# Kernel optimization log

Hardware: AMD Instinct MI355X
Metric: run time of the kernel (lower is better)

The kernel has to match this reference:

```python
import jax, jax.numpy as jnp
import numpy as np

B, N, D = 2, 2048, 1024
H = 16
HD = D // H  # 64
N_CTX = 256


def setup_inputs() -> dict:
    key = jax.random.key(0)
    ks = jax.random.split(key, 10)
    x = jax.random.normal(ks[0], (B, N, D), dtype=jnp.float32)
    ctx_ppr = jax.random.uniform(ks[1], (N_CTX,), dtype=jnp.float32, minval=1e-4, maxval=1.0)
    ctx_trust = jax.random.uniform(ks[2], (N_CTX,), dtype=jnp.float32)
    attn_mask = jax.random.randint(ks[3], (N, N), 0, 2).astype(jnp.bool_)
    # parameters (nn.Linear convention: y = x @ W.T + b)
    s_in = 1.0 / np.sqrt(D)
    W_in = jax.random.uniform(ks[4], (3 * D, D), dtype=jnp.float32, minval=-s_in, maxval=s_in)
    b_in = jax.random.uniform(ks[5], (3 * D,), dtype=jnp.float32, minval=-s_in, maxval=s_in)
    W_out = jax.random.uniform(ks[6], (D, D), dtype=jnp.float32, minval=-s_in, maxval=s_in)
    b_out = jax.random.uniform(ks[7], (D,), dtype=jnp.float32, minval=-s_in, maxval=s_in)
    log_ppr_alpha = jnp.ones((1,), jnp.float32) * 0.1
    trust_scale = jnp.ones((1,), jnp.float32) * 0.1
    return {"x": x, "ctx_ppr": ctx_ppr, "ctx_trust": ctx_trust, "n_ctx": N_CTX,
            "attn_mask": attn_mask, "W_in": W_in, "b_in": b_in,
            "W_out": W_out, "b_out": b_out,
            "log_ppr_alpha": log_ppr_alpha, "trust_scale": trust_scale}


def reference(x, ctx_ppr, ctx_trust, n_ctx, attn_mask, W_in, b_in, W_out, b_out,
              log_ppr_alpha, trust_scale):
    Bx, Nx, Dx = x.shape
    scale = HD ** -0.5
    qkv = x @ W_in.T + b_in  # [B,N,3D]
    q, k, v = jnp.split(qkv, 3, axis=-1)
    q = q.reshape(Bx, Nx, H, HD).transpose(0, 2, 1, 3)  # [B,H,N,d]
    k = k.reshape(Bx, Nx, H, HD).transpose(0, 2, 1, 3)
    v = v.reshape(Bx, Nx, H, HD).transpose(0, 2, 1, 3)
    if n_ctx > 0:
        gate = jax.nn.sigmoid(trust_scale[0] * ctx_trust)  # [n_ctx]
        gate_full = jnp.concatenate([gate, jnp.ones(Nx - n_ctx, x.dtype)])
        v = v * gate_full[None, None, :, None]
    logits = jnp.einsum('bhqd,bhkd->bhqk', q, k) * scale
    if n_ctx > 0:
        bias = log_ppr_alpha[0] * jnp.log(jnp.clip(ctx_ppr, 1e-8, None))
        col_bias = jnp.concatenate([bias, jnp.zeros(Nx - n_ctx, x.dtype)])
        logits = logits + col_bias[None, None, None, :]
    logits = jnp.where(attn_mask[None, None, :, :], -jnp.inf, logits)
    weights = jax.nn.softmax(logits, axis=-1)
    out = jnp.einsum('bhqk,bhkd->bhqd', weights, v)
    out = out.transpose(0, 2, 1, 3).reshape(Bx, Nx, Dx)
    return out @ W_out.T + b_out
```

## Files before the change

kernel.cpp:

```cpp
#include <hip/hip_runtime.h>
#include <hip/hip_bf16.h>
#include <math.h>

#define B_   2
#define N_   2048
#define D_   1024
#define H_   16
#define TD_  3072
#define LOG2E 1.44269504088896340736f
#define SCALE_Q (0.125f * LOG2E)

typedef short  bf16x8 __attribute__((ext_vector_type(8)));
typedef _Float16 f16x8 __attribute__((ext_vector_type(8)));
typedef float  f32x4  __attribute__((ext_vector_type(4)));
typedef float  f32x16 __attribute__((ext_vector_type(16)));

#define MFMA16(a, b, c)   __builtin_amdgcn_mfma_f32_16x16x32_bf16(a, b, c, 0, 0, 0)
#define MFMA32B(a, b, c)  __builtin_amdgcn_mfma_f32_32x32x16_bf16(a, b, c, 0, 0, 0)
#define MFMA32H(a, b, c)  __builtin_amdgcn_mfma_f32_32x32x16_f16(a, b, c, 0, 0, 0)

__device__ __forceinline__ ushort f2bf(float f) {
    union { float f; unsigned u; } v; v.f = f;
    unsigned r = (v.u + 0x7fffu + ((v.u >> 16) & 1u)) >> 16;
    return (ushort)r;
}
__device__ __forceinline__ unsigned pkrtz(float a, float b) {
    typedef __fp16 h2 __attribute__((ext_vector_type(2)));
    union { h2 h; unsigned u; } c;
    c.h = __builtin_amdgcn_cvt_pkrtz(a, b);
    return c.u;
}
__device__ __forceinline__ void async16(const void* g, void* l) {
    __builtin_amdgcn_global_load_lds(
        (const __attribute__((address_space(1))) unsigned*)g,
        (__attribute__((address_space(3))) unsigned*)l, 16, 0, 0);
}

__global__ __launch_bounds__(256) void preprocess(
    const float* __restrict__ x, const float* __restrict__ W_in,
    const float* __restrict__ W_out, const float* __restrict__ ctx_ppr,
    const float* __restrict__ log_alpha, const int* __restrict__ n_ctx_p,
    const int* __restrict__ mask,
    ushort* __restrict__ xb, ushort* __restrict__ wib, ushort* __restrict__ wob,
    float* __restrict__ biasrow, unsigned* __restrict__ maskbits)
{
    const int J0 = 1048576, J1 = 786432, J2 = 262144, JM = 131072, JB = 2048;
    int t = blockIdx.x * 256 + threadIdx.x;
    if (t < J0 + J1 + J2) {
        const float* src; ushort* dst; int i = t;
        if (i < J0)           { src = x;      dst = xb;  }
        else if (i < J0 + J1) { i -= J0;      src = W_in;  dst = wib; }
        else                  { i -= J0 + J1; src = W_out; dst = wob; }
        float4 v = ((const float4*)src)[i];
        ushort4 o;
        o.x = f2bf(v.x); o.y = f2bf(v.y); o.z = f2bf(v.z); o.w = f2bf(v.w);
        ((ushort4*)dst)[i] = o;
    } else if (t < J0 + J1 + J2 + JM) {
        int i = t - (J0 + J1 + J2);
        const int4* m = (const int4*)(mask + (size_t)i * 32);
        unsigned bits = 0u;
        #pragma unroll
        for (int j = 0; j < 8; ++j) {
            int4 w = m[j];
            bits |= (w.x != 0 ? 1u : 0u) << (j * 4 + 0);
            bits |= (w.y != 0 ? 1u : 0u) << (j * 4 + 1);
            bits |= (w.z != 0 ? 1u : 0u) << (j * 4 + 2);
            bits |= (w.w != 0 ? 1u : 0u) << (j * 4 + 3);
        }
        maskbits[i] = bits;
    } else if (t < J0 + J1 + J2 + JM + JB) {
        int k = t - (J0 + J1 + J2 + JM);
        int nc = n_ctx_p[0];
        float bv = 0.f;
        if (k < nc) bv = log_alpha[0] * __log2f(fmaxf(ctx_ppr[k], 1e-8f));
        biasrow[k] = bv;
    }
}

template<int BCOL, int MODE>
__global__ __launch_bounds__(256) void gemm_bt(
    const ushort* __restrict__ A, const ushort* __restrict__ Bw,
    const float* __restrict__ bias, float* __restrict__ Cout,
    ushort* __restrict__ qkout, _Float16* __restrict__ vTout,
    int Ncol, int K,
    const float* __restrict__ ctx_trust, const float* __restrict__ trust_scale,
    const int* __restrict__ n_ctx_p)
{
    constexpr int NT = BCOL / 32;
    __shared__ ushort tA[128 * 32];
    __shared__ ushort tB[BCOL * 32];
    const int tid = threadIdx.x;
    const int lane = tid & 63, wv = tid >> 6;
    const int ln = lane & 15, kg = lane >> 4;
    const int rh = wv >> 1, ch = wv & 1;
    const int row0 = blockIdx.y * 128, col0 = blockIdx.x * BCOL;

    int offA[4], offB[NT];
    #pragma unroll
    for (int i = 0; i < 4; ++i) {
        int ra = rh * 64 + i * 16 + ln;
        offA[i] = ra * 32 + ((kg ^ ((ra >> 1) & 3)) << 3);
    }
    #pragma unroll
    for (int i = 0; i < NT; ++i) {
        int rb = ch * (BCOL / 2) + i * 16 + ln;
        offB[i] = rb * 32 + ((kg ^ ((rb >> 1) & 3)) << 3);
    }
    f32x4 acc[4][NT];
    #pragma unroll
    for (int i = 0; i < 4; ++i)
        #pragma unroll
        for (int j = 0; j < NT; ++j) acc[i][j] = (f32x4){0.f, 0.f, 0.f, 0.f};

    for (int kt = 0; kt < K; kt += 32) {
        __syncthreads();
        #pragma unroll
        for (int r2 = 0; r2 < 2; ++r2) {
            int g = r2 * 256 + tid;
            int row = g >> 2;
            int srck = ((g & 3) ^ ((row >> 1) & 3)) << 3;
            async16(A + (size_t)(row0 + row) * K + kt + srck, &tA[g * 8]);
        }
        #pragma unroll
        for (int r2 = 0; r2 < BCOL / 64; ++r2) {
            int g = r2 * 256 + tid;
            int row = g >> 2;
            int srck = ((g & 3) ^ ((row >> 1) & 3)) << 3;
            async16(Bw + (size_t)(col0 + row) * K + kt + srck, &tB[g * 8]);
        }
        __syncthreads();
        bf16x8 af[4], bfr[NT];
        #pragma unroll
        for (int i = 0; i < 4; ++i)  af[i]  = *(const bf16x8*)&tA[offA[i]];
        #pragma unroll
        for (int i = 0; i < NT; ++i) bfr[i] = *(const bf16x8*)&tB[offB[i]];
        #pragma unroll
        for (int mt = 0; mt < 4; ++mt)
            #pragma unroll
            for (int nt = 0; nt < NT; ++nt)
                acc[mt][nt] = MFMA16(af[mt], bfr[nt], acc[mt][nt]);
    }

    const int nctx = n_ctx_p ? n_ctx_p[0] : 0;
    const float ts = trust_scale ? trust_scale[0] : 0.f;
    #pragma unroll
    for (int nt = 0; nt < NT; ++nt) {
        int col = col0 + ch * (BCOL / 2) + nt * 16 + ln;
        float bv = bias[col];
        #pragma unroll
        for (int mt = 0; mt < 4; ++mt) {
            int rbase = row0 + rh * 64 + mt * 16 + kg * 4;
            f32x4 a = acc[mt][nt];
            if (MODE == 0) {
                #pragma unroll
                for (int reg = 0; reg < 4; ++reg)
                    Cout[(size_t)(rbase + reg) * Ncol + col] = a[reg] + bv;
            } else {
                if (col < D_) {
                    #pragma unroll
                    for (int reg = 0; reg < 4; ++reg)
                        qkout[(size_t)(rbase + reg) * 2048 + col] =
                            f2bf((a[reg] + bv) * SCALE_Q);
                } else if (col < 2 * D_) {
                    #pragma unroll
                    for (int reg = 0; reg < 4; ++reg)
                        qkout[(size_t)(rbase + reg) * 2048 + col] = f2bf(a[reg] + bv);
                } else {
                    int vc = col - 2 * D_;
                    int hh = vc >> 6, dim = vc & 63;
                    int bb = rbase >> 11, nbase = rbase & (N_ - 1);
                    ushort4 o;
                    #pragma unroll
                    for (int reg = 0; reg < 4; ++reg) {
                        float v = a[reg] + bv;
                        int n = nbase + reg;
                        if (n < nctx) {
                            float g = 1.f / (1.f + __expf(-ts * ctx_trust[n]));
                            v *= g;
                        }
                        _Float16 hv = (_Float16)v;
                        ((ushort*)&o)[reg] = *(ushort*)&hv;
                    }
                    *(ushort4*)&vTout[((size_t)(bb * 16 + hh) * 64 + dim) * 2048 + nbase] = o;
                }
            }
        }
    }
}

__global__ __launch_bounds__(256) void attn(
    const ushort* __restrict__ qkb,
    const _Float16* __restrict__ vT,
    const unsigned* __restrict__ maskbits,
    const float* __restrict__ biasrow,
    const int* __restrict__ n_ctx_p,
    ushort* __restrict__ attb)
{
    __shared__ ushort   Kt[2][64 * 64];
    __shared__ _Float16 Vt[2][64 * 64];
    const int tid = threadIdx.x;
    const int lane = tid & 63, wv = tid >> 6;
    const int q31 = lane & 31, hi = lane >> 5;
    const int b = blockIdx.y >> 4, h = blockIdx.y & 15;
    const int q0w = blockIdx.x * 128 + wv * 32;
    const int nctx = n_ctx_p[0];

    bf16x8 qf[4];
    {
        const ushort* qrow = qkb + (size_t)(b * N_ + q0w + q31) * 2048 + h * 64;
        #pragma unroll
        for (int ks = 0; ks < 4; ++ks)
            qf[ks] = *(const bf16x8*)(qrow + ks * 16 + hi * 8);
    }
    const size_t kgbase = (size_t)(b * N_) * 2048 + 1024 + h * 64;
    const _Float16* vbase = vT + (size_t)((b * 16 + h) * 64) * 2048;

    f32x16 O[2];
    O[0] = (f32x16)(0.f); O[1] = (f32x16)(0.f);
    float lrun = 0.f;

    {
        #pragma unroll
        for (int r2 = 0; r2 < 2; ++r2) {
            int g = r2 * 256 + tid; int row = g >> 3; int sg = (g & 7) ^ (row & 7);
            async16(qkb + kgbase + (size_t)row * 2048 + sg * 8, &Kt[0][g * 8]);
        }
        #pragma unroll
        for (int r2 = 0; r2 < 2; ++r2) {
            int g = r2 * 256 + tid; int row = g >> 3; int sg = (g & 7) ^ (row & 7);
            async16(vbase + (size_t)row * 2048 + sg * 8, &Vt[0][g * 8]);
        }
    }

    const int swz = q31 & 7;
    for (int ci = 0; ci < 32; ++ci) {
        const int c0 = ci * 64;
        __syncthreads();
        if (ci < 31) {
            const int c1 = c0 + 64, nb = (ci + 1) & 1;
            #pragma unroll
            for (int r2 = 0; r2 < 2; ++r2) {
                int g = r2 * 256 + tid; int row = g >> 3; int sg = (g & 7) ^ (row & 7);
                async16(qkb + kgbase + (size_t)(c1 + row) * 2048 + sg * 8, &Kt[nb][g * 8]);
            }
            #pragma unroll
            for (int r2 = 0; r2 < 2; ++r2) {
                int g = r2 * 256 + tid; int row = g >> 3; int sg = (g & 7) ^ (row & 7);
                async16(vbase + (size_t)row * 2048 + c1 + sg * 8, &Vt[nb][g * 8]);
            }
        }
        const ushort*   KT = Kt[ci & 1];
        const _Float16* VT = Vt[ci & 1];

        f32x16 S[2];
        S[0] = (f32x16)(0.f); S[1] = (f32x16)(0.f);
        #pragma unroll
        for (int t = 0; t < 2; ++t) {
            const int rbase = (t * 32 + q31) * 64;
            #pragma unroll
            for (int ks = 0; ks < 4; ++ks) {
                bf16x8 kf = *(const bf16x8*)&KT[rbase + (((ks * 2 + hi) ^ swz) << 3)];
                S[t] = MFMA32B(kf, qf[ks], S[t]);
            }
        }

        uint2 mw = *(const uint2*)&maskbits[(size_t)(q0w + q31) * 64 + ci * 2];
        unsigned msh[2] = { mw.x >> (hi * 4), mw.y >> (hi * 4) };
        unsigned pk[2][8];
        float lsum = 0.f;
        const bool has_bias = (c0 < nctx);
        #pragma unroll
        for (int t = 0; t < 2; ++t) {
            float p[16];
            #pragma unroll
            for (int g = 0; g < 4; ++g) {
                f32x4 bb = (f32x4){0.f, 0.f, 0.f, 0.f};
                if (has_bias)
                    bb = *(const f32x4*)&biasrow[c0 + t * 32 + g * 8 + hi * 4];
                #pragma unroll
                for (int r = 0; r < 4; ++r) {
                    const int reg = g * 4 + r;
                    const int br = r + 8 * g;
                    float s = S[t][reg] + bb[r] - 4.f;
                    s = ((msh[t] >> br) & 1u) ? -1e30f : s;
                    p[reg] = __builtin_exp2f(s);
                }
            }
            float l0 = (p[0] + p[1]) + (p[2] + p[3]);
            float l1 = (p[4] + p[5]) + (p[6] + p[7]);
            float l2 = (p[8] + p[9]) + (p[10] + p[11]);
            float l3 = (p[12] + p[13]) + (p[14] + p[15]);
            lsum += (l0 + l1) + (l2 + l3);
            #pragma unroll
            for (int i = 0; i < 8; ++i)
                pk[t][i] = pkrtz(p[2 * i], p[2 * i + 1]);
        }
        lrun += lsum;

        #pragma unroll
        for (int ks = 0; ks < 4; ++ks) {
            const int t = ks >> 1, lo4 = (ks & 1) * 4;
            unsigned u0 = pk[t][lo4 + 0], u1 = pk[t][lo4 + 1];
            unsigned u2 = pk[t][lo4 + 2], u3 = pk[t][lo4 + 3];
            unsigned own0 = hi ? u2 : u0, own1 = hi ? u3 : u1;
            unsigned snd0 = hi ? u0 : u2, snd1 = hi ? u1 : u3;
            unsigned rv0 = (unsigned)__shfl_xor((int)snd0, 32);
            unsigned rv1 = (unsigned)__shfl_xor((int)snd1, 32);
            union { f16x8 v; unsigned u[4]; } frag;
            frag.u[0] = hi ? rv0 : own0;
            frag.u[1] = hi ? rv1 : own1;
            frag.u[2] = hi ? own0 : rv0;
            frag.u[3] = hi ? own1 : rv1;
            #pragma unroll
            for (int t2 = 0; t2 < 2; ++t2) {
                const int vb = (t2 * 32 + q31) * 64;
                union { f16x8 v; int4 i; } vf;
                vf.i = *(const int4*)&VT[vb + (((ks * 2 + hi) ^ swz) << 3)];
                O[t2] = MFMA32H(vf.v, frag.v, O[t2]);
            }
        }
    }

    float l = lrun + __shfl_xor(lrun, 32);
    float inv = 1.f / l;
    ushort* orow = attb + (size_t)(b * N_ + q0w + q31) * 1024 + h * 64;
    #pragma unroll
    for (int t = 0; t < 2; ++t)
        #pragma unroll
        for (int g = 0; g < 4; ++g) {
            ushort4 o;
            #pragma unroll
            for (int r = 0; r < 4; ++r)
                ((ushort*)&o)[r] = f2bf(O[t][g * 4 + r] * inv);
            *(ushort4*)&orow[t * 32 + g * 8 + hi * 4] = o;
        }
}

extern "C" void kernel_launch(void* const* d_in, const int* in_sizes, int n_in,
                              void* d_out, int out_size, void* d_ws, size_t ws_size,
                              hipStream_t stream)
{
    const float* x         = (const float*)d_in[0];
    const float* ctx_ppr   = (const float*)d_in[1];
    const float* ctx_trust = (const float*)d_in[2];
    const int*   n_ctx_p   = (const int*)d_in[3];
    const int*   attn_mask = (const int*)d_in[4];
    const float* W_in      = (const float*)d_in[5];
    const float* b_in      = (const float*)d_in[6];
    const float* W_out     = (const float*)d_in[7];
    const float* b_out     = (const float*)d_in[8];
    const float* log_alpha = (const float*)d_in[9];
    const float* trust_sc  = (const float*)d_in[10];
    float* out = (float*)d_out;

    char* ws = (char*)d_ws;
    ushort*    xb       = (ushort*)ws;    ws += (size_t)4096 * 1024 * 2;
    ushort*    wib      = (ushort*)ws;    ws += (size_t)3072 * 1024 * 2;
    ushort*    wob      = (ushort*)ws;    ws += (size_t)1024 * 1024 * 2;
    ushort*    qkb      = (ushort*)ws;    ws += (size_t)4096 * 2048 * 2;
    _Float16*  vT       = (_Float16*)ws;  ws += (size_t)2048 * 2048 * 2;
    ushort*    attbuf   = (ushort*)ws;    ws += (size_t)4096 * 1024 * 2;
    float*     biasrow  = (float*)ws;     ws += 2048 * 4;
    unsigned*  maskbits = (unsigned*)ws;  ws += (size_t)2048 * 64 * 4;

    hipLaunchKernelGGL(preprocess, dim3(8712), dim3(256), 0, stream,
                       x, W_in, W_out, ctx_ppr, log_alpha, n_ctx_p, attn_mask,
                       xb, wib, wob, biasrow, maskbits);

    hipLaunchKernelGGL((gemm_bt<128, 1>), dim3(24, 32), dim3(256), 0, stream,
                       xb, wib, b_in, (float*)nullptr, qkb, vT, TD_, 1024,
                       ctx_trust, trust_sc, n_ctx_p);

    hipLaunchKernelGGL(attn, dim3(16, 32), dim3(256), 0, stream,
                       qkb, vT, maskbits, biasrow, n_ctx_p, attbuf);

    hipLaunchKernelGGL((gemm_bt<64, 0>), dim3(16, 32), dim3(256), 0, stream,
                       attbuf, wob, b_out, out, (ushort*)nullptr, (_Float16*)nullptr,
                       1024, 1024, ctx_trust, trust_sc, n_ctx_p);
}
```

Measured before the change: 268.5 us.

## Precompute dense mask-bias term, split V GEMM transposed, shrink attention blocks

The bit-packed mask and separate bias row are replaced by a dense fp32 term matrix that folds bias, mask and the -4 offset together, so the attention inner loop only adds and exponentiates. V is produced by a separate transposed GEMM (W_v times x) that writes the vT layout with coalesced stores. The attention kernel moves to 128-thread blocks with a new LDS swizzle and accumulates the row sum in half2 from the packed probabilities. The cost is a 16MB fp32 term buffer that must be written and then re-read per head, plus lower-precision softmax denominators.

```diff
diff --git a/kernel.cpp b/kernel.cpp
--- a/kernel.cpp
+++ b/kernel.cpp
@@ -1,5 +1,6 @@
 #include <hip/hip_runtime.h>
 #include <hip/hip_bf16.h>
+#include <hip/hip_fp16.h>
 #include <math.h>
 
 #define B_   2
@@ -42,9 +43,9 @@
     const float* __restrict__ log_alpha, const int* __restrict__ n_ctx_p,
     const int* __restrict__ mask,
     ushort* __restrict__ xb, ushort* __restrict__ wib, ushort* __restrict__ wob,
-    float* __restrict__ biasrow, unsigned* __restrict__ maskbits)
+    float* __restrict__ term)
 {
-    const int J0 = 1048576, J1 = 786432, J2 = 262144, JM = 131072, JB = 2048;
+    const int J0 = 1048576, J1 = 786432, J2 = 262144, JT = 1048576;
     int t = blockIdx.x * 256 + threadIdx.x;
     if (t < J0 + J1 + J2) {
         const float* src; ushort* dst; int i = t;
@@ -55,34 +56,32 @@
         ushort4 o;
         o.x = f2bf(v.x); o.y = f2bf(v.y); o.z = f2bf(v.z); o.w = f2bf(v.w);
         ((ushort4*)dst)[i] = o;
-    } else if (t < J0 + J1 + J2 + JM) {
+    } else if (t < J0 + J1 + J2 + JT) {
         int i = t - (J0 + J1 + J2);
-        const int4* m = (const int4*)(mask + (size_t)i * 32);
-        unsigned bits = 0u;
-        #pragma unroll
-        for (int j = 0; j < 8; ++j) {
-            int4 w = m[j];
-            bits |= (w.x != 0 ? 1u : 0u) << (j * 4 + 0);
-            bits |= (w.y != 0 ? 1u : 0u) << (j * 4 + 1);
-            bits |= (w.z != 0 ? 1u : 0u) << (j * 4 + 2);
-            bits |= (w.w != 0 ? 1u : 0u) << (j * 4 + 3);
-        }
-        maskbits[i] = bits;
-    } else if (t < J0 + J1 + J2 + JM + JB) {
-        int k = t - (J0 + J1 + J2 + JM);
+        int k4 = (i & 511) * 4;
+        int4 m = ((const int4*)mask)[i];
         int nc = n_ctx_p[0];
-        float bv = 0.f;
-        if (k < nc) bv = log_alpha[0] * __log2f(fmaxf(ctx_ppr[k], 1e-8f));
-        biasrow[k] = bv;
+        float al = log_alpha[0];
+        float4 o;
+        float bv[4];
+        #pragma unroll
+        for (int j = 0; j < 4; ++j) {
+            int k = k4 + j;
+            bv[j] = (k < nc) ? (al * __log2f(fmaxf(ctx_ppr[k], 1e-8f)) - 4.f) : -4.f;
+        }
+        o.x = m.x ? -1e30f : bv[0];
+        o.y = m.y ? -1e30f : bv[1];
+        o.z = m.z ? -1e30f : bv[2];
+        o.w = m.w ? -1e30f : bv[3];
+        ((float4*)term)[i] = o;
     }
 }
 
 template<int BCOL, int MODE>
 __global__ __launch_bounds__(256) void gemm_bt(
     const ushort* __restrict__ A, const ushort* __restrict__ Bw,
-    const float* __restrict__ bias, float* __restrict__ Cout,
-    ushort* __restrict__ qkout, _Float16* __restrict__ vTout,
-    int Ncol, int K,
+    const float* __restrict__ bias, float* __restrict__ Cf,
+    ushort* __restrict__ Ch, int Ncol, int K,
     const float* __restrict__ ctx_trust, const float* __restrict__ trust_scale,
     const int* __restrict__ n_ctx_p)
 {
@@ -146,7 +145,13 @@
     #pragma unroll
     for (int nt = 0; nt < NT; ++nt) {
         int col = col0 + ch * (BCOL / 2) + nt * 16 + ln;
-        float bv = bias[col];
+        float cbv = (MODE != 2) ? bias[col] : 0.f;
+        float gmul = 1.f;
+        if (MODE == 2) {
+            int tok = col & (N_ - 1);
+            if (tok < nctx)
+                gmul = 1.f / (1.f + __expf(-ts * ctx_trust[tok]));
+        }
         #pragma unroll
         for (int mt = 0; mt < 4; ++mt) {
             int rbase = row0 + rh * 64 + mt * 16 + kg * 4;
@@ -154,46 +159,30 @@
             if (MODE == 0) {
                 #pragma unroll
                 for (int reg = 0; reg < 4; ++reg)
-                    Cout[(size_t)(rbase + reg) * Ncol + col] = a[reg] + bv;
+                    Cf[(size_t)(rbase + reg) * Ncol + col] = a[reg] + cbv;
+            } else if (MODE == 1) {
+                const float qs = (col < D_) ? SCALE_Q : 1.f;
+                #pragma unroll
+                for (int reg = 0; reg < 4; ++reg)
+                    Ch[(size_t)(rbase + reg) * Ncol + col] = f2bf((a[reg] + cbv) * qs);
             } else {
-                if (col < D_) {
-                    #pragma unroll
-                    for (int reg = 0; reg < 4; ++reg)
-                        qkout[(size_t)(rbase + reg) * 2048 + col] =
-                            f2bf((a[reg] + bv) * SCALE_Q);
-                } else if (col < 2 * D_) {
-                    #pragma unroll
-                    for (int reg = 0; reg < 4; ++reg)
-                        qkout[(size_t)(rbase + reg) * 2048 + col] = f2bf(a[reg] + bv);
-                } else {
-                    int vc = col - 2 * D_;
-                    int hh = vc >> 6, dim = vc & 63;
-                    int bb = rbase >> 11, nbase = rbase & (N_ - 1);
-                    ushort4 o;
-                    #pragma unroll
-                    for (int reg = 0; reg < 4; ++reg) {
-                        float v = a[reg] + bv;
-                        int n = nbase + reg;
-                        if (n < nctx) {
-                            float g = 1.f / (1.f + __expf(-ts * ctx_trust[n]));
-                            v *= g;
-                        }
-                        _Float16 hv = (_Float16)v;
-                        ((ushort*)&o)[reg] = *(ushort*)&hv;
-                    }
-                    *(ushort4*)&vTout[((size_t)(bb * 16 + hh) * 64 + dim) * 2048 + nbase] = o;
+                f32x4 bv4 = *(const f32x4*)&bias[rbase];
+                #pragma unroll
+                for (int reg = 0; reg < 4; ++reg) {
+                    float v = (a[reg] + bv4[reg]) * gmul;
+                    _Float16 hv = (_Float16)v;
+                    union { _Float16 h; ushort u; } cv; cv.h = hv;
+                    Ch[((size_t)((col >> 11) * 1024 + rbase + reg)) * 2048 + (col & (N_ - 1))] = cv.u;
                 }
             }
         }
     }
 }
 
-__global__ __launch_bounds__(256) void attn(
+__global__ __launch_bounds__(128) void attn(
     const ushort* __restrict__ qkb,
     const _Float16* __restrict__ vT,
-    const unsigned* __restrict__ maskbits,
-    const float* __restrict__ biasrow,
-    const int* __restrict__ n_ctx_p,
+    const float* __restrict__ term,
     ushort* __restrict__ attb)
 {
     __shared__ ushort   Kt[2][64 * 64];
@@ -201,57 +190,73 @@
     const int tid = threadIdx.x;
     const int lane = tid & 63, wv = tid >> 6;
     const int q31 = lane & 31, hi = lane >> 5;
-    const int b = blockIdx.y >> 4, h = blockIdx.y & 15;
-    const int q0w = blockIdx.x * 128 + wv * 32;
-    const int nctx = n_ctx_p[0];
+    const int bh = blockIdx.x;
+    const int b = bh >> 4, h = bh & 15;
+    const int q = blockIdx.y * 64 + wv * 32 + q31;
 
     bf16x8 qf[4];
     {
-        const ushort* qrow = qkb + (size_t)(b * N_ + q0w + q31) * 2048 + h * 64;
+        const ushort* qrow = qkb + (size_t)(b * N_ + q) * 2048 + h * 64;
         #pragma unroll
         for (int ks = 0; ks < 4; ++ks)
             qf[ks] = *(const bf16x8*)(qrow + ks * 16 + hi * 8);
     }
     const size_t kgbase = (size_t)(b * N_) * 2048 + 1024 + h * 64;
-    const _Float16* vbase = vT + (size_t)((b * 16 + h) * 64) * 2048;
+    const _Float16* vbase = vT + (size_t)(b * 1024 + h * 64) * 2048;
+    const float* trow = term + (size_t)q * 2048;
 
     f32x16 O[2];
     O[0] = (f32x16)(0.f); O[1] = (f32x16)(0.f);
     float lrun = 0.f;
 
-    {
-        #pragma unroll
-        for (int r2 = 0; r2 < 2; ++r2) {
-            int g = r2 * 256 + tid; int row = g >> 3; int sg = (g & 7) ^ (row & 7);
-            async16(qkb + kgbase + (size_t)row * 2048 + sg * 8, &Kt[0][g * 8]);
-        }
-        #pragma unroll
-        for (int r2 = 0; r2 < 2; ++r2) {
-            int g = r2 * 256 + tid; int row = g >> 3; int sg = (g & 7) ^ (row & 7);
-            async16(vbase + (size_t)row * 2048 + sg * 8, &Vt[0][g * 8]);
-        }
-    }
-
-    const int swz = q31 & 7;
+    #pragma unroll
+    for (int r2 = 0; r2 < 4; ++r2) {
+        int g = r2 * 128 + tid; int row = g >> 3;
+        int sg = (g & 7) ^ ((row ^ (row >> 3)) & 7);
+        async16(qkb + kgbase + (size_t)row * 2048 + sg * 8, &Kt[0][g * 8]);
+    }
+    #pragma unroll
+    for (int r2 = 0; r2 < 4; ++r2) {
+        int g = r2 * 128 + tid; int row = g >> 3;
+        int sg = (g & 7) ^ ((row ^ (row >> 3)) & 7);
+        async16(vbase + (size_t)row * 2048 + sg * 8, &Vt[0][g * 8]);
+    }
+
+    int fsw[2];
+    #pragma unroll
+    for (int t = 0; t < 2; ++t) {
+        int row = t * 32 + q31;
+        fsw[t] = (row ^ (row >> 3)) & 7;
+    }
+
     for (int ci = 0; ci < 32; ++ci) {
         const int c0 = ci * 64;
         __syncthreads();
         if (ci < 31) {
             const int c1 = c0 + 64, nb = (ci + 1) & 1;
             #pragma unroll
-            for (int r2 = 0; r2 < 2; ++r2) {
-                int g = r2 * 256 + tid; int row = g >> 3; int sg = (g & 7) ^ (row & 7);
+            for (int r2 = 0; r2 < 4; ++r2) {
+                int g = r2 * 128 + tid; int row = g >> 3;
+                int sg = (g & 7) ^ ((row ^ (row >> 3)) & 7);
                 async16(qkb + kgbase + (size_t)(c1 + row) * 2048 + sg * 8, &Kt[nb][g * 8]);
             }
             #pragma unroll
-            for (int r2 = 0; r2 < 2; ++r2) {
-                int g = r2 * 256 + tid; int row = g >> 3; int sg = (g & 7) ^ (row & 7);
+            for (int r2 = 0; r2 < 4; ++r2) {
+                int g = r2 * 128 + tid; int row = g >> 3;
+                int sg = (g & 7) ^ ((row ^ (row >> 3)) & 7);
                 async16(vbase + (size_t)row * 2048 + c1 + sg * 8, &Vt[nb][g * 8]);
             }
         }
         const ushort*   KT = Kt[ci & 1];
         const _Float16* VT = Vt[ci & 1];
 
+        f32x4 tm[2][4];
+        #pragma unroll
+        for (int t = 0; t < 2; ++t)
+            #pragma unroll
+            for (int g = 0; g < 4; ++g)
+                tm[t][g] = *(const f32x4*)(trow + c0 + t * 32 + g * 8 + hi * 4);
+
         f32x16 S[2];
         S[0] = (f32x16)(0.f); S[1] = (f32x16)(0.f);
         #pragma unroll
@@ -259,43 +264,34 @@
             const int rbase = (t * 32 + q31) * 64;
             #pragma unroll
             for (int ks = 0; ks < 4; ++ks) {
-                bf16x8 kf = *(const bf16x8*)&KT[rbase + (((ks * 2 + hi) ^ swz) << 3)];
+                bf16x8 kf = *(const bf16x8*)&KT[rbase + (((ks * 2 + hi) ^ fsw[t]) << 3)];
                 S[t] = MFMA32B(kf, qf[ks], S[t]);
             }
         }
 
-        uint2 mw = *(const uint2*)&maskbits[(size_t)(q0w + q31) * 64 + ci * 2];
-        unsigned msh[2] = { mw.x >> (hi * 4), mw.y >> (hi * 4) };
         unsigned pk[2][8];
-        float lsum = 0.f;
-        const bool has_bias = (c0 < nctx);
+        __half2 hs0 = __float2half2_rn(0.f), hs1 = __float2half2_rn(0.f);
         #pragma unroll
         for (int t = 0; t < 2; ++t) {
             float p[16];
             #pragma unroll
-            for (int g = 0; g < 4; ++g) {
-                f32x4 bb = (f32x4){0.f, 0.f, 0.f, 0.f};
-                if (has_bias)
-                    bb = *(const f32x4*)&biasrow[c0 + t * 32 + g * 8 + hi * 4];
+            for (int g = 0; g < 4; ++g)
                 #pragma unroll
                 for (int r = 0; r < 4; ++r) {
                     const int reg = g * 4 + r;
-                    const int br = r + 8 * g;
-                    float s = S[t][reg] + bb[r] - 4.f;
-                    s = ((msh[t] >> br) & 1u) ? -1e30f : s;
-                    p[reg] = __builtin_exp2f(s);
+                    p[reg] = __builtin_exp2f(S[t][reg] + tm[t][g][r]);
                 }
-            }
-            float l0 = (p[0] + p[1]) + (p[2] + p[3]);
-            float l1 = (p[4] + p[5]) + (p[6] + p[7]);
-            float l2 = (p[8] + p[9]) + (p[10] + p[11]);
-            float l3 = (p[12] + p[13]) + (p[14] + p[15]);
-            lsum += (l0 + l1) + (l2 + l3);
-            #pragma unroll
-            for (int i = 0; i < 8; ++i)
+            #pragma unroll
+            for (int i = 0; i < 8; ++i) {
                 pk[t][i] = pkrtz(p[2 * i], p[2 * i + 1]);
-        }
-        lrun += lsum;
+                union { unsigned u; __half2 h; } c; c.u = pk[t][i];
+                if (i & 1) hs1 = __hadd2(hs1, c.h); else hs0 = __hadd2(hs0, c.h);
+            }
+        }
+        {
+            __half2 hs = __hadd2(hs0, hs1);
+            lrun += __low2float(hs) + __high2float(hs);
+        }
 
         #pragma unroll
         for (int ks = 0; ks < 4; ++ks) {
@@ -315,7 +311,7 @@
             for (int t2 = 0; t2 < 2; ++t2) {
                 const int vb = (t2 * 32 + q31) * 64;
                 union { f16x8 v; int4 i; } vf;
-                vf.i = *(const int4*)&VT[vb + (((ks * 2 + hi) ^ swz) << 3)];
+                vf.i = *(const int4*)&VT[vb + (((ks * 2 + hi) ^ fsw[t2]) << 3)];
                 O[t2] = MFMA32H(vf.v, frag.v, O[t2]);
             }
         }
@@ -323,7 +319,7 @@
 
     float l = lrun + __shfl_xor(lrun, 32);
     float inv = 1.f / l;
-    ushort* orow = attb + (size_t)(b * N_ + q0w + q31) * 1024 + h * 64;
+    ushort* orow = attb + (size_t)(b * N_ + q) * 1024 + h * 64;
     #pragma unroll
     for (int t = 0; t < 2; ++t)
         #pragma unroll
@@ -354,27 +350,30 @@
     float* out = (float*)d_out;
 
     char* ws = (char*)d_ws;
-    ushort*    xb       = (ushort*)ws;    ws += (size_t)4096 * 1024 * 2;
-    ushort*    wib      = (ushort*)ws;    ws += (size_t)3072 * 1024 * 2;
-    ushort*    wob      = (ushort*)ws;    ws += (size_t)1024 * 1024 * 2;
-    ushort*    qkb      = (ushort*)ws;    ws += (size_t)4096 * 2048 * 2;
-    _Float16*  vT       = (_Float16*)ws;  ws += (size_t)2048 * 2048 * 2;
-    ushort*    attbuf   = (ushort*)ws;    ws += (size_t)4096 * 1024 * 2;
-    float*     biasrow  = (float*)ws;     ws += 2048 * 4;
-    unsigned*  maskbits = (unsigned*)ws;  ws += (size_t)2048 * 64 * 4;
-
-    hipLaunchKernelGGL(preprocess, dim3(8712), dim3(256), 0, stream,
+    ushort*    xb     = (ushort*)ws;    ws += (size_t)4096 * 1024 * 2;
+    ushort*    wib    = (ushort*)ws;    ws += (size_t)3072 * 1024 * 2;
+    ushort*    wob    = (ushort*)ws;    ws += (size_t)1024 * 1024 * 2;
+    ushort*    qkb    = (ushort*)ws;    ws += (size_t)4096 * 2048 * 2;
+    _Float16*  vT     = (_Float16*)ws;  ws += (size_t)2048 * 2048 * 2;
+    ushort*    attbuf = (ushort*)ws;    ws += (size_t)4096 * 1024 * 2;
+    float*     term   = (float*)ws;     ws += (size_t)2048 * 2048 * 4;
+
+    hipLaunchKernelGGL(preprocess, dim3(12288), dim3(256), 0, stream,
                        x, W_in, W_out, ctx_ppr, log_alpha, n_ctx_p, attn_mask,
-                       xb, wib, wob, biasrow, maskbits);
-
-    hipLaunchKernelGGL((gemm_bt<128, 1>), dim3(24, 32), dim3(256), 0, stream,
-                       xb, wib, b_in, (float*)nullptr, qkb, vT, TD_, 1024,
-                       ctx_trust, trust_sc, n_ctx_p);
-
-    hipLaunchKernelGGL(attn, dim3(16, 32), dim3(256), 0, stream,
-                       qkb, vT, maskbits, biasrow, n_ctx_p, attbuf);
+                       xb, wib, wob, term);
+
+    hipLaunchKernelGGL((gemm_bt<128, 1>), dim3(16, 32), dim3(256), 0, stream,
+                       xb, wib, b_in, (float*)nullptr, qkb, 2048, 1024,
+                       (const float*)nullptr, (const float*)nullptr, (const int*)nullptr);
+
+    hipLaunchKernelGGL((gemm_bt<64, 2>), dim3(64, 8), dim3(256), 0, stream,
+                       wib + (size_t)2048 * 1024, xb, b_in + 2 * D_, (float*)nullptr,
+                       (ushort*)vT, 4096, 1024, ctx_trust, trust_sc, n_ctx_p);
+
+    hipLaunchKernelGGL(attn, dim3(32, 32), dim3(128), 0, stream,
+                       qkb, vT, term, attbuf);
 
     hipLaunchKernelGGL((gemm_bt<64, 0>), dim3(16, 32), dim3(256), 0, stream,
-                       attbuf, wob, b_out, out, (ushort*)nullptr, (_Float16*)nullptr,
-                       1024, 1024, ctx_trust, trust_sc, n_ctx_p);
-}
+                       attbuf, wob, b_out, out, (ushort*)nullptr, 1024, 1024,
+                       (const float*)nullptr, (const float*)nullptr, (const int*)nullptr);
+}
```

Result: slower. 288.7 us (+7.6%).
